# Performance work log

Measured on AMD Instinct MI355X. Metric: run time of the kernel, lower is better.

Reference implementation:

```python
import jax, jax.numpy as jnp
import numpy as np

WD, WH, WW = 2, 7, 7          # window size (d, h, w)
N = WD * WH * WW              # 98 tokens per window
DIM = 768
NH = 24
HD = DIM // NH                # 32
SCALE = HD ** -0.5
NW = 64                       # windows per image
B = 4
B_ = B * NW                   # 256


def _relative_position_index():
    d, h, w = np.meshgrid(np.arange(WD), np.arange(WH), np.arange(WW), indexing='ij')
    coords = np.stack([d.ravel(), h.ravel(), w.ravel()])        # (3, N)
    rel = (coords[:, :, None] - coords[:, None, :]).transpose(1, 2, 0)  # (N, N, 3)
    rel = rel + np.array([WD - 1, WH - 1, WW - 1])
    rel = rel * np.array([(2 * WH - 1) * (2 * WW - 1), 2 * WW - 1, 1])
    return rel.sum(-1).astype(np.int32)                         # (N, N)


def setup_inputs() -> dict:
    key = jax.random.key(0)
    ks = jax.random.split(key, 5)
    table_rows = (2 * WD - 1) * (2 * WH - 1) * (2 * WW - 1)     # 507
    return {
        'x': jax.random.normal(ks[0], (B_, N, DIM), jnp.float32),
        'mask': jax.random.normal(ks[1], (NW, N, N), jnp.float32),
        'qkv_w': jax.random.normal(ks[2], (3 * DIM, DIM), jnp.float32) * 0.02,
        'qkv_b': jax.random.normal(ks[3], (3 * DIM,), jnp.float32) * 0.02,
        'rel_table': jax.random.normal(ks[4], (table_rows, NH), jnp.float32) * 0.02,
        'rel_index': jnp.asarray(_relative_position_index()),
    }


def reference(x, mask, qkv_w, qkv_b, rel_table, rel_index):
    Bs, n, c = x.shape
    # qkv linear; einops '(nH hD qkv)' => last dim factored as (nH, hD, 3)
    qkv = x @ qkv_w.T + qkv_b                                   # (Bs, N, 3C)
    qkv = qkv.reshape(Bs, n, NH, HD, 3)
    q, k, v = (jnp.moveaxis(qkv, -1, 0)                         # (3, Bs, N, nH, hD)
                  .transpose(0, 1, 3, 2, 4))                    # (3, Bs, nH, N, hD)
    attn = jnp.einsum('bhqd,bhkd->bhqk', q, k) * SCALE          # (Bs, nH, N, N)
    bias = rel_table[rel_index]                                 # (N, N, nH)
    attn = attn + bias.transpose(2, 0, 1)[None]                 # + (1, nH, N, N)
    # window mask add
    attn = attn.reshape(Bs // NW, NW, NH, n, n) + mask[None, :, None]
    attn = attn.reshape(Bs, NH, n, n)
    attn = jax.nn.softmax(attn, axis=-1)
    out = jnp.einsum('bhqk,bhkd->bhqd', attn, v)                # (Bs, nH, N, hD)
    return out.transpose(0, 2, 1, 3).reshape(Bs, n, c)          # (Bs, N, C)
```

## Files before the change

kernel.cpp:

```cpp
#include <hip/hip_runtime.h>
#include <hip/hip_bf16.h>
#include <stdint.h>


#define NTOK 98
#define MT 7
#define NPAD 112
#define DIMX 768
#define NHEAD 24
#define HDIM 32
#define NQKV 2304
#define BROWS 25088
#define SCALE 0.17677669529663689f
#define LOG2E 1.4426950408889634f
#define SCL2E (SCALE * LOG2E)
#define NN2 (NTOK * NTOK)
#define BMROW 112
#define BMSZ (BMROW * BMROW)

#define NB_X 18816
#define NB_W 1728
#define NB_BM 18816

#if __has_builtin(__builtin_amdgcn_exp2f)
#define EXP2F(x) __builtin_amdgcn_exp2f(x)
#else
#define EXP2F(x) exp2f(x)
#endif

typedef __attribute__((ext_vector_type(8))) short short8;
typedef __attribute__((ext_vector_type(4))) short short4v;
typedef __attribute__((ext_vector_type(4))) float floatx4;

__device__ __forceinline__ short f2b(float f) {
    __hip_bfloat16 h = __float2bfloat16(f);
    return __builtin_bit_cast(short, h);
}
__device__ __forceinline__ float b2f(unsigned short s) {
    return __builtin_bit_cast(float, ((unsigned)s) << 16);
}

__device__ __forceinline__ void gload_lds16(const void* g, void* l) {
    __builtin_amdgcn_global_load_lds(
        (const __attribute__((address_space(1))) void*)g,
        (__attribute__((address_space(3))) void*)l, 16, 0, 0);
}

__device__ __forceinline__ void bm_body(int t,
                                        const float* __restrict__ rel_table,
                                        const int* __restrict__ rel_index,
                                        const float* __restrict__ mask,
                                        short* __restrict__ bm) {
    int wh = t / (BMSZ / 4);
    int r4 = t % (BMSZ / 4);
    int i = r4 / 28;
    int j0 = (r4 % 28) * 4;
    int h = wh % NHEAD, w = wh / NHEAD;
    short4v o;
    #pragma unroll
    for (int jj = 0; jj < 4; ++jj) {
        int j = j0 + jj;
        float val = -1e30f;
        if (i < NTOK && j < NTOK) {
            float bv = rel_table[(size_t)rel_index[i * NTOK + j] * NHEAD + h];
            float mv = mask[(size_t)w * NN2 + i * NTOK + j];
            val = (bv + mv) * LOG2E;
        }
        o[jj] = f2b(val);
    }
    *(short4v*)(bm + (size_t)wh * BMSZ + i * BMROW + j0) = o;
}

__global__ void prep_kernel(const float* __restrict__ x,
                            const float* __restrict__ w,
                            const float* __restrict__ rel_table,
                            const int* __restrict__ rel_index,
                            const float* __restrict__ mask,
                            short* __restrict__ xb,
                            short* __restrict__ wb,
                            short* __restrict__ bm) {
    int bid = blockIdx.x;
    if (bid < NB_X) {
        int i = bid * 256 + threadIdx.x;
        float4 f = ((const float4*)x)[i];
        short4v s = { f2b(f.x), f2b(f.y), f2b(f.z), f2b(f.w) };
        ((short4v*)xb)[i] = s;
    } else if (bid < NB_X + NB_W) {
        int i = (bid - NB_X) * 256 + threadIdx.x;
        int cp = i / 192, k4 = i % 192;
        int s = cp / DIMX, rem = cp % DIMX;
        int orig = (rem >> 5) * 96 + (rem & 31) * 3 + s;
        float sc = (s == 0) ? SCL2E : 1.0f;
        float4 f = ((const float4*)(w + (size_t)orig * DIMX))[k4];
        short4v o = { f2b(f.x * sc), f2b(f.y * sc), f2b(f.z * sc), f2b(f.w * sc) };
        ((short4v*)(wb + (size_t)cp * DIMX))[k4] = o;
    } else {
        int t = (bid - NB_X - NB_W) * 256 + threadIdx.x;
        bm_body(t, rel_table, rel_index, mask, bm);
    }
}

__global__ void bm_kernel(const float* __restrict__ rel_table,
                          const int* __restrict__ rel_index,
                          const float* __restrict__ mask,
                          short* __restrict__ bm) {
    int t = blockIdx.x * 256 + threadIdx.x;
    if (t >= 64 * NHEAD * BMSZ / 4) return;
    bm_body(t, rel_table, rel_index, mask, bm);
}

__global__ void bias_gather_kernel(const float* __restrict__ rel_table,
                                   const int* __restrict__ rel_index,
                                   float* __restrict__ bias_pre) {
    int t = blockIdx.x * 256 + threadIdx.x;
    if (t >= NHEAD * NN2) return;
    int h  = t / NN2;
    int ij = t % NN2;
    bias_pre[t] = rel_table[(size_t)rel_index[ij] * NHEAD + h];
}

__global__ void gemm_kernel(const short* __restrict__ xb,
                            const short* __restrict__ wb,
                            const float* __restrict__ qkv_b,
                            short* __restrict__ qkv) {
    __shared__ short At[128 * 64];
    __shared__ short Bt[128 * 64];
    const int tid  = threadIdx.x;
    const int lane = tid & 63;
    const int wv   = tid >> 6;
    const int wr   = wv >> 1, wc = wv & 1;
    const int l15  = lane & 15;
    const int l4   = lane >> 4;

    int bid = blockIdx.x;
    int swz = (bid & 7) * 441 + (bid >> 3);
    const int mtile = swz / 18;
    const int ntile = swz % 18;

    const short* aB = xb + (size_t)(mtile * 128) * DIMX;
    const short* bB = wb + (size_t)(ntile * 128) * DIMX;
    const int lrow = lane >> 3;
    const int lcs  = (((lane & 7) ^ lrow) * 8);
    const int sa   = (l15 & 7) << 3;

    floatx4 acc[4][4];
    #pragma unroll
    for (int m = 0; m < 4; ++m)
        #pragma unroll
        for (int n = 0; n < 4; ++n) acc[m][n] = (floatx4){0.f, 0.f, 0.f, 0.f};

    for (int kb = 0; kb < 12; ++kb) {
        #pragma unroll
        for (int j = 0; j < 4; ++j) {
            int r = wv * 32 + j * 8;
            gload_lds16(aB + (size_t)(r + lrow) * DIMX + kb * 64 + lcs, &At[r * 64]);
            gload_lds16(bB + (size_t)(r + lrow) * DIMX + kb * 64 + lcs, &Bt[r * 64]);
        }
        __syncthreads();
        #pragma unroll
        for (int kh = 0; kh < 2; ++kh) {
            int k0 = kh * 32 + l4 * 8;
            int k0s = k0 ^ sa;
            short8 af[4], bfr[4];
            #pragma unroll
            for (int m = 0; m < 4; ++m)
                af[m] = *(const short8*)(&At[(wr * 64 + m * 16 + l15) * 64 + k0s]);
            #pragma unroll
            for (int n = 0; n < 4; ++n)
                bfr[n] = *(const short8*)(&Bt[(wc * 64 + n * 16 + l15) * 64 + k0s]);
            #pragma unroll
            for (int m = 0; m < 4; ++m)
                #pragma unroll
                for (int n = 0; n < 4; ++n)
                    acc[m][n] = __builtin_amdgcn_mfma_f32_16x16x32_bf16(
                        af[m], bfr[n], acc[m][n], 0, 0, 0);
        }
        __syncthreads();
    }

    #pragma unroll
    for (int n = 0; n < 4; ++n) {
        int col = ntile * 128 + wc * 64 + n * 16 + l15;
        int s = col / DIMX, rem = col % DIMX;
        int orig = (rem >> 5) * 96 + (rem & 31) * 3 + s;
        float bias = qkv_b[orig] * ((s == 0) ? SCL2E : 1.0f);
        #pragma unroll
        for (int m = 0; m < 4; ++m) {
            int row0 = mtile * 128 + wr * 64 + m * 16 + l4 * 4;
            #pragma unroll
            for (int r = 0; r < 4; ++r)
                qkv[(size_t)(row0 + r) * NQKV + col] = f2b(acc[m][n][r] + bias);
        }
    }
}

struct __align__(16) SMemC {
    short P[NPAD * 128];
    short q[NPAD * HDIM];
    short k[NPAD * HDIM];
    short vt[HDIM * 128];
};

__global__ __launch_bounds__(256, 3) void attn_kernel4(
    const short* __restrict__ qkv,
    const short* __restrict__ bm,
    float* __restrict__ out) {
    __shared__ SMemC sm;
    const int tid  = threadIdx.x;
    const int lane = tid & 63;
    const int wv   = tid >> 6;
    const int l15  = lane & 15;
    const int l4   = lane >> 4;
    int id = blockIdx.x;
    int nb = (id & 7) * 768 + (id >> 3);
    const int b = nb / NHEAD;
    const int h = nb % NHEAD;
    const short* qbase = qkv + (size_t)b * NTOK * NQKV;

    #pragma unroll
    for (int it = 0; it < 2; ++it) {
        int row0 = it * 64 + wv * 16;
        if (row0 < NTOK) {
            int row = row0 + (lane >> 2);
            int seg = (lane & 3) * 8;
            if (row < NTOK) {
                gload_lds16(qbase + (size_t)row * NQKV + h * HDIM + seg,
                            &sm.q[row0 * HDIM]);
                gload_lds16(qbase + (size_t)row * NQKV + DIMX + h * HDIM + seg,
                            &sm.k[row0 * HDIM]);
            }
        }
    }
    if (tid < 196) {
        int t = (tid >> 2) * 2, dh = tid & 3;
        const short* vp = qbase + (size_t)t * NQKV + 2 * DIMX + h * HDIM + dh * 8;
        short8 va = *(const short8*)vp;
        short8 vb = *(const short8*)(vp + NQKV);
        #pragma unroll
        for (int j = 0; j < 8; ++j) {
            int d = dh * 8 + j;
            int csw = t ^ ((d & 7) << 3);
            unsigned pk = ((unsigned)(unsigned short)vb[j] << 16) |
                          (unsigned)(unsigned short)va[j];
            *(unsigned*)(&sm.vt[d * 128 + csw]) = pk;
        }
    }
    if (tid < 112) {
        int a = tid / 56, r2 = (tid % 56) >> 2, seg = (tid & 3) * 8;
        short* dst = (a ? sm.k : sm.q) + (NTOK + r2) * HDIM + seg;
        *(uint4*)dst = (uint4){0u, 0u, 0u, 0u};
    }
    for (int t = tid; t < HDIM * 30; t += 256) {
        int d = t / 30, c = NTOK + t % 30;
        sm.vt[d * 128 + (c ^ ((d & 7) << 3))] = 0;
    }
    for (int t = tid; t < NPAD * 16; t += 256) {
        int r = t >> 4, c = 112 + (t & 15);
        sm.P[r * 128 + (c ^ ((r & 7) << 3))] = 0;
    }
    __syncthreads();

    int mt[2];
    mt[0] = wv;
    mt[1] = (wv + 4 < MT) ? (wv + 4) : wv;

    floatx4 sacc[2][7];
    #pragma unroll
    for (int i = 0; i < 2; ++i)
        #pragma unroll
        for (int j = 0; j < 7; ++j) sacc[i][j] = (floatx4){0.f, 0.f, 0.f, 0.f};
    {
        int k0 = l4 * 8;
        short8 bq[2];
        #pragma unroll
        for (int iq = 0; iq < 2; ++iq)
            bq[iq] = *(const short8*)(&sm.q[(mt[iq] * 16 + l15) * HDIM + k0]);
        #pragma unroll
        for (int kt = 0; kt < 7; ++kt) {
            short8 ak = *(const short8*)(&sm.k[(kt * 16 + l15) * HDIM + k0]);
            #pragma unroll
            for (int iq = 0; iq < 2; ++iq)
                sacc[iq][kt] = __builtin_amdgcn_mfma_f32_16x16x32_bf16(
                    ak, bq[iq], sacc[iq][kt], 0, 0, 0);
        }
    }

    const short* bmh = bm + ((size_t)(b & 63) * NHEAD + h) * BMSZ;
    const int swzp = (l15 & 7) << 3;

    #pragma unroll
    for (int iq = 0; iq < 2; ++iq) {
        int q = mt[iq] * 16 + l15;
        const short* bmq = bmh + q * BMROW + l4 * 4;
        float vv[7][4];
        #pragma unroll
        for (int kt = 0; kt < 7; ++kt) {
            short4v bm4 = *(const short4v*)(bmq + kt * 16);
            #pragma unroll
            for (int r = 0; r < 4; ++r)
                vv[kt][r] = sacc[iq][kt][r] + b2f((unsigned short)bm4[r]);
        }
        float mx = vv[0][0];
        #pragma unroll
        for (int kt = 0; kt < 7; ++kt)
            #pragma unroll
            for (int r = 0; r < 4; ++r) mx = fmaxf(mx, vv[kt][r]);
        mx = fmaxf(mx, __shfl_xor(mx, 16));
        mx = fmaxf(mx, __shfl_xor(mx, 32));
        float s = 0.f;
        #pragma unroll
        for (int kt = 0; kt < 7; ++kt)
            #pragma unroll
            for (int r = 0; r < 4; ++r) {
                float e = EXP2F(vv[kt][r] - mx);
                vv[kt][r] = e;
                s += e;
            }
        s += __shfl_xor(s, 16);
        s += __shfl_xor(s, 32);
        float inv = (q < NTOK) ? 1.f / s : 0.f;
        #pragma unroll
        for (int kt = 0; kt < 7; ++kt) {
            short4v pw = { f2b(vv[kt][0] * inv), f2b(vv[kt][1] * inv),
                           f2b(vv[kt][2] * inv), f2b(vv[kt][3] * inv) };
            *(short4v*)(&sm.P[q * 128 + ((kt * 16 + l4 * 4) ^ swzp)]) = pw;
        }
    }
    __syncthreads();

    floatx4 oacc[2][2];
    #pragma unroll
    for (int i = 0; i < 2; ++i)
        #pragma unroll
        for (int j = 0; j < 2; ++j) oacc[i][j] = (floatx4){0.f, 0.f, 0.f, 0.f};

    #pragma unroll
    for (int kt = 0; kt < 4; ++kt) {
        int kk = (kt * 32 + l4 * 8) ^ swzp;
        short8 ap[2];
        #pragma unroll
        for (int im = 0; im < 2; ++im)
            ap[im] = *(const short8*)(&sm.P[(mt[im] * 16 + l15) * 128 + kk]);
        #pragma unroll
        for (int nt = 0; nt < 2; ++nt) {
            short8 bv = *(const short8*)(&sm.vt[(nt * 16 + l15) * 128 + kk]);
            #pragma unroll
            for (int im = 0; im < 2; ++im)
                oacc[im][nt] = __builtin_amdgcn_mfma_f32_16x16x32_bf16(
                    ap[im], bv, oacc[im][nt], 0, 0, 0);
        }
    }

    float* ob = out + (size_t)b * NTOK * DIMX + h * HDIM;
    #pragma unroll
    for (int im = 0; im < 2; ++im)
        #pragma unroll
        for (int nt = 0; nt < 2; ++nt) {
            int dd = nt * 16 + l15;
            #pragma unroll
            for (int r = 0; r < 4; ++r) {
                int tok = mt[im] * 16 + l4 * 4 + r;
                if (tok < NTOK)
                    ob[(size_t)tok * DIMX + dd] = oacc[im][nt][r];
            }
        }
}

struct __align__(16) SMemF {
    union {
        struct {
            short xt[NPAD * 64];
            short wt[96 * 64];
        } p1;
        short P[NPAD * 128];
    } u;
    short q[NPAD * HDIM];
    short k[NPAD * HDIM];
    short vt[HDIM * 128];
};

__global__ __launch_bounds__(256, 3) void attn_fused(
    const float* __restrict__ x,
    const float* __restrict__ mask,
    const float* __restrict__ qkv_w,
    const float* __restrict__ qkv_b,
    const float* __restrict__ bias_pre,
    const float* __restrict__ rel_table,
    const int* __restrict__ rel_index,
    float* __restrict__ out) {
    __shared__ SMemF sm;
    const int tid  = threadIdx.x;
    const int lane = tid & 63;
    const int wv   = tid >> 6;
    const int l15  = lane & 15;
    const int l4   = lane >> 4;
    const int b = blockIdx.x / NHEAD;
    const int h = blockIdx.x % NHEAD;
    const float* xp = x + (size_t)b * NTOK * DIMX;
    const float* wp = qkv_w + (size_t)h * 96 * DIMX;
    int mt[2];
    mt[0] = wv;
    mt[1] = (wv + 4 < MT) ? (wv + 4) : wv;

    floatx4 acc[2][6];
    #pragma unroll
    for (int i = 0; i < 2; ++i)
        #pragma unroll
        for (int j = 0; j < 6; ++j) acc[i][j] = (floatx4){0.f, 0.f, 0.f, 0.f};

    for (int kb = 0; kb < 12; ++kb) {
        for (int t = tid; t < NTOK * 16; t += 256) {
            int row = t >> 4, c = t & 15;
            float4 f = *(const float4*)(xp + (size_t)row * DIMX + kb * 64 + c * 4);
            short4v s = { f2b(f.x), f2b(f.y), f2b(f.z), f2b(f.w) };
            *(short4v*)(&sm.u.p1.xt[row * 64 + c * 4]) = s;
        }
        for (int t = tid; t < 96 * 16; t += 256) {
            int row = t >> 4, c = t & 15;
            float4 f = *(const float4*)(wp + (size_t)row * DIMX + kb * 64 + c * 4);
            short4v s = { f2b(f.x), f2b(f.y), f2b(f.z), f2b(f.w) };
            *(short4v*)(&sm.u.p1.wt[row * 64 + c * 4]) = s;
        }
        if (tid < 14 * 8) {
            int row = 98 + (tid >> 3), c = tid & 7;
            uint4 z = {0u, 0u, 0u, 0u};
            *(uint4*)(&sm.u.p1.xt[row * 64 + c * 8]) = z;
        }
        __syncthreads();
        #pragma unroll
        for (int ks = 0; ks < 2; ++ks) {
            int k0 = ks * 32 + l4 * 8;
            short8 aM[2];
            #pragma unroll
            for (int im = 0; im < 2; ++im)
                aM[im] = *(const short8*)(&sm.u.p1.xt[(mt[im] * 16 + l15) * 64 + k0]);
            #pragma unroll
            for (int nt = 0; nt < 6; ++nt) {
                short8 bN = *(const short8*)(&sm.u.p1.wt[(nt * 16 + l15) * 64 + k0]);
                #pragma unroll
                for (int im = 0; im < 2; ++im)
                    acc[im][nt] = __builtin_amdgcn_mfma_f32_16x16x32_bf16(
                        aM[im], bN, acc[im][nt], 0, 0, 0);
            }
        }
        __syncthreads();
    }

    #pragma unroll
    for (int im = 0; im < 2; ++im)
        #pragma unroll
        for (int nt = 0; nt < 6; ++nt) {
            int col = nt * 16 + l15;
            int d = col / 3, s = col % 3;
            float bias = qkv_b[h * 96 + col];
            #pragma unroll
            for (int r = 0; r < 4; ++r) {
                int tok = mt[im] * 16 + l4 * 4 + r;
                short val = f2b(acc[im][nt][r] + bias);
                if (s == 0)      sm.q[tok * HDIM + d] = val;
                else if (s == 1) sm.k[tok * HDIM + d] = val;
                else             sm.vt[d * 128 + tok] = val;
            }
        }
    __syncthreads();
    for (int t = tid; t < HDIM * 30; t += 256) {
        int d = t / 30, c = 98 + t % 30;
        sm.vt[d * 128 + c] = 0;
    }
    for (int t = tid; t < NPAD * 16; t += 256) {
        int row = t >> 4, c = 112 + (t & 15);
        sm.u.P[row * 128 + c] = 0;
    }

    floatx4 sacc[2][7];
    #pragma unroll
    for (int i = 0; i < 2; ++i)
        #pragma unroll
        for (int j = 0; j < 7; ++j) sacc[i][j] = (floatx4){0.f, 0.f, 0.f, 0.f};
    {
        int k0 = l4 * 8;
        short8 aq[2];
        #pragma unroll
        for (int im = 0; im < 2; ++im)
            aq[im] = *(const short8*)(&sm.q[(mt[im] * 16 + l15) * HDIM + k0]);
        #pragma unroll
        for (int nt = 0; nt < 7; ++nt) {
            short8 bk = *(const short8*)(&sm.k[(nt * 16 + l15) * HDIM + k0]);
            #pragma unroll
            for (int im = 0; im < 2; ++im)
                sacc[im][nt] = __builtin_amdgcn_mfma_f32_16x16x32_bf16(
                    aq[im], bk, sacc[im][nt], 0, 0, 0);
        }
    }

    const float* biash = bias_pre ? (bias_pre + (size_t)h * NN2) : nullptr;
    const size_t moff = (size_t)(b & 63) * NN2;

    #pragma unroll
    for (int im = 0; im < 2; ++im)
        #pragma unroll
        for (int r = 0; r < 4; ++r) {
            int row = mt[im] * 16 + l4 * 4 + r;
            bool vrow = row < NTOK;
            float v[7];
            #pragma unroll
            for (int nt = 0; nt < 7; ++nt) {
                int j = nt * 16 + l15;
                bool vj = vrow && (j < NTOK);
                float bmv = 0.f;
                if (vj) {
                    float bias = biash ? biash[row * NTOK + j]
                        : rel_table[(size_t)rel_index[row * NTOK + j] * NHEAD + h];
                    bmv = bias + mask[moff + row * NTOK + j];
                }
                v[nt] = vj ? sacc[im][nt][r] * SCALE + bmv : -1e30f;
            }
            float mx = v[0];
            #pragma unroll
            for (int nt = 1; nt < 7; ++nt) mx = fmaxf(mx, v[nt]);
            #pragma unroll
            for (int off = 1; off < 16; off <<= 1) mx = fmaxf(mx, __shfl_xor(mx, off));
            float s = 0.f;
            #pragma unroll
            for (int nt = 0; nt < 7; ++nt) {
                float e = (v[nt] > -1e29f) ? __expf(v[nt] - mx) : 0.f;
                v[nt] = e;
                s += e;
            }
            #pragma unroll
            for (int off = 1; off < 16; off <<= 1) s += __shfl_xor(s, off);
            float inv = vrow ? 1.f / s : 0.f;
            #pragma unroll
            for (int nt = 0; nt < 7; ++nt)
                sm.u.P[row * 128 + nt * 16 + l15] = f2b(v[nt] * inv);
        }
    __syncthreads();

    floatx4 oacc[2][2];
    #pragma unroll
    for (int i = 0; i < 2; ++i)
        #pragma unroll
        for (int j = 0; j < 2; ++j) oacc[i][j] = (floatx4){0.f, 0.f, 0.f, 0.f};
    #pragma unroll
    for (int kt = 0; kt < 4; ++kt) {
        int kk = kt * 32 + l4 * 8;
        short8 ap[2];
        #pragma unroll
        for (int im = 0; im < 2; ++im)
            ap[im] = *(const short8*)(&sm.u.P[(mt[im] * 16 + l15) * 128 + kk]);
        #pragma unroll
        for (int nt = 0; nt < 2; ++nt) {
            short8 bv = *(const short8*)(&sm.vt[(nt * 16 + l15) * 128 + kk]);
            #pragma unroll
            for (int im = 0; im < 2; ++im)
                oacc[im][nt] = __builtin_amdgcn_mfma_f32_16x16x32_bf16(
                    ap[im], bv, oacc[im][nt], 0, 0, 0);
        }
    }
    float* ob = out + (size_t)b * NTOK * DIMX + h * HDIM;
    #pragma unroll
    for (int im = 0; im < 2; ++im)
        #pragma unroll
        for (int nt = 0; nt < 2; ++nt) {
            int dd = nt * 16 + l15;
            #pragma unroll
            for (int r = 0; r < 4; ++r) {
                int tok = mt[im] * 16 + l4 * 4 + r;
                if (tok < NTOK)
                    ob[(size_t)tok * DIMX + dd] = oacc[im][nt][r];
            }
        }
}

extern "C" void kernel_launch(void* const* d_in, const int* in_sizes, int n_in,
                              void* d_out, int out_size, void* d_ws, size_t ws_size,
                              hipStream_t stream) {
    const float* x = (const float*)d_in[0];
    const float* mask = (const float*)d_in[1];
    const float* qkv_w = (const float*)d_in[2];
    const float* qkv_b = (const float*)d_in[3];
    const float* rel_table = (const float*)d_in[4];
    const int* rel_index = (const int*)d_in[5];
    for (int i = 0; i < n_in; ++i) {
        switch (in_sizes[i]) {
            case 256 * NTOK * DIMX:  x         = (const float*)d_in[i]; break;
            case 64 * NN2:           mask      = (const float*)d_in[i]; break;
            case 3 * DIMX * DIMX:    qkv_w     = (const float*)d_in[i]; break;
            case 3 * DIMX:           qkv_b     = (const float*)d_in[i]; break;
            case 507 * NHEAD:        rel_table = (const float*)d_in[i]; break;
            case NN2:                rel_index = (const int*)d_in[i]; break;
            default: break;
        }
    }
    float* out = (float*)d_out;

    const size_t xb_bytes   = (size_t)BROWS * DIMX * 2;
    const size_t wb_bytes   = (size_t)NQKV * DIMX * 2;
    const size_t qkv_bytes  = (size_t)BROWS * NQKV * 2;
    const size_t bm_bytes   = (size_t)64 * NHEAD * BMSZ * 2;
    const size_t total      = xb_bytes + wb_bytes + qkv_bytes;

    if (ws_size >= total) {
        short* xb  = (short*)d_ws;
        short* wb  = (short*)((char*)d_ws + xb_bytes);
        short* qkv = (short*)((char*)d_ws + xb_bytes + wb_bytes);

        if (ws_size >= total + bm_bytes) {
            short* bmp = (short*)((char*)d_ws + total);
            prep_kernel<<<NB_X + NB_W + NB_BM, 256, 0, stream>>>(
                x, qkv_w, rel_table, rel_index, mask, xb, wb, bmp);
            gemm_kernel<<<196 * 18, 256, 0, stream>>>(xb, wb, qkv_b, qkv);
            attn_kernel4<<<256 * NHEAD, 256, 0, stream>>>(qkv, bmp, out);
        } else {
            short* bmp = (short*)d_ws;
            prep_kernel<<<NB_X + NB_W, 256, 0, stream>>>(
                x, qkv_w, rel_table, rel_index, mask, xb, wb, nullptr);
            gemm_kernel<<<196 * 18, 256, 0, stream>>>(xb, wb, qkv_b, qkv);
            int nbm = 64 * NHEAD * BMSZ / 4;
            bm_kernel<<<(nbm + 255) / 256, 256, 0, stream>>>(
                rel_table, rel_index, mask, bmp);
            attn_kernel4<<<256 * NHEAD, 256, 0, stream>>>(qkv, bmp, out);
        }
    } else {
        const size_t bias_bytes = (size_t)NHEAD * NN2 * sizeof(float);
        float* bias_pre = (ws_size >= bias_bytes) ? (float*)d_ws : nullptr;
        if (bias_pre) {
            int nb = NHEAD * NN2;
            bias_gather_kernel<<<(nb + 255) / 256, 256, 0, stream>>>(rel_table, rel_index, bias_pre);
        }
        attn_fused<<<256 * NHEAD, 256, 0, stream>>>(x, mask, qkv_w, qkv_b,
                                                    bias_pre, rel_table, rel_index, out);
    }
}
```

Measured before the change: 347.2 us.

## Store QKV head-planar, fold bias-mask build into GEMM launch, raise MFMA priority

The GEMM epilogue now writes Q, K and V into per-head contiguous planes (s, head, row, d) instead of interleaved rows of width 2304. The attention kernel therefore loads each head's 98x32 tile as contiguous memory, replacing strided row gathers. The bias+mask table build moves from the prep kernel into extra blocks of the GEMM launch, so it runs alongside the GEMM tiles. s_setprio is raised around the MFMA loops in attention. The risk is that the epilogue stores now stride 64 bytes per row, which may coalesce worse, and the GEMM tail may be lengthened by the bm blocks.

```diff
diff --git a/kernel.cpp b/kernel.cpp
--- a/kernel.cpp
+++ b/kernel.cpp
@@ -17,10 +17,12 @@
 #define NN2 (NTOK * NTOK)
 #define BMROW 112
 #define BMSZ (BMROW * BMROW)
+#define PLANE ((size_t)BROWS * HDIM)
 
 #define NB_X 18816
 #define NB_W 1728
 #define NB_BM 18816
+#define GEMM_BLKS 3528
 
 #if __has_builtin(__builtin_amdgcn_exp2f)
 #define EXP2F(x) __builtin_amdgcn_exp2f(x)
@@ -73,19 +75,15 @@
 
 __global__ void prep_kernel(const float* __restrict__ x,
                             const float* __restrict__ w,
-                            const float* __restrict__ rel_table,
-                            const int* __restrict__ rel_index,
-                            const float* __restrict__ mask,
                             short* __restrict__ xb,
-                            short* __restrict__ wb,
-                            short* __restrict__ bm) {
+                            short* __restrict__ wb) {
     int bid = blockIdx.x;
     if (bid < NB_X) {
         int i = bid * 256 + threadIdx.x;
         float4 f = ((const float4*)x)[i];
         short4v s = { f2b(f.x), f2b(f.y), f2b(f.z), f2b(f.w) };
         ((short4v*)xb)[i] = s;
-    } else if (bid < NB_X + NB_W) {
+    } else {
         int i = (bid - NB_X) * 256 + threadIdx.x;
         int cp = i / 192, k4 = i % 192;
         int s = cp / DIMX, rem = cp % DIMX;
@@ -94,9 +92,6 @@
         float4 f = ((const float4*)(w + (size_t)orig * DIMX))[k4];
         short4v o = { f2b(f.x * sc), f2b(f.y * sc), f2b(f.z * sc), f2b(f.w * sc) };
         ((short4v*)(wb + (size_t)cp * DIMX))[k4] = o;
-    } else {
-        int t = (bid - NB_X - NB_W) * 256 + threadIdx.x;
-        bm_body(t, rel_table, rel_index, mask, bm);
     }
 }
 
@@ -122,7 +117,16 @@
 __global__ void gemm_kernel(const short* __restrict__ xb,
                             const short* __restrict__ wb,
                             const float* __restrict__ qkv_b,
-                            short* __restrict__ qkv) {
+                            short* __restrict__ qkv,
+                            const float* __restrict__ rel_table,
+                            const int* __restrict__ rel_index,
+                            const float* __restrict__ mask,
+                            short* __restrict__ bm) {
+    if (blockIdx.x >= GEMM_BLKS) {
+        int t = (blockIdx.x - GEMM_BLKS) * 256 + threadIdx.x;
+        bm_body(t, rel_table, rel_index, mask, bm);
+        return;
+    }
     __shared__ short At[128 * 64];
     __shared__ short Bt[128 * 64];
     const int tid  = threadIdx.x;
@@ -182,14 +186,16 @@
     for (int n = 0; n < 4; ++n) {
         int col = ntile * 128 + wc * 64 + n * 16 + l15;
         int s = col / DIMX, rem = col % DIMX;
-        int orig = (rem >> 5) * 96 + (rem & 31) * 3 + s;
+        int h2 = rem >> 5, d = rem & 31;
+        int orig = h2 * 96 + d * 3 + s;
         float bias = qkv_b[orig] * ((s == 0) ? SCL2E : 1.0f);
+        short* base = qkv + (size_t)(s * NHEAD + h2) * PLANE + d;
         #pragma unroll
         for (int m = 0; m < 4; ++m) {
             int row0 = mtile * 128 + wr * 64 + m * 16 + l4 * 4;
             #pragma unroll
             for (int r = 0; r < 4; ++r)
-                qkv[(size_t)(row0 + r) * NQKV + col] = f2b(acc[m][n][r] + bias);
+                base[(size_t)(row0 + r) * HDIM] = f2b(acc[m][n][r] + bias);
         }
     }
 }
@@ -201,7 +207,7 @@
     short vt[HDIM * 128];
 };
 
-__global__ __launch_bounds__(256, 3) void attn_kernel4(
+__global__ __launch_bounds__(256, 3) void attn_kernel5(
     const short* __restrict__ qkv,
     const short* __restrict__ bm,
     float* __restrict__ out) {
@@ -215,27 +221,25 @@
     int nb = (id & 7) * 768 + (id >> 3);
     const int b = nb / NHEAD;
     const int h = nb % NHEAD;
-    const short* qbase = qkv + (size_t)b * NTOK * NQKV;
+    const short* qh = qkv + (size_t)h * PLANE            + (size_t)b * NTOK * HDIM;
+    const short* kh = qkv + (size_t)(NHEAD + h) * PLANE  + (size_t)b * NTOK * HDIM;
+    const short* vh = qkv + (size_t)(2 * NHEAD + h) * PLANE + (size_t)b * NTOK * HDIM;
 
     #pragma unroll
     for (int it = 0; it < 2; ++it) {
         int row0 = it * 64 + wv * 16;
         if (row0 < NTOK) {
-            int row = row0 + (lane >> 2);
-            int seg = (lane & 3) * 8;
-            if (row < NTOK) {
-                gload_lds16(qbase + (size_t)row * NQKV + h * HDIM + seg,
-                            &sm.q[row0 * HDIM]);
-                gload_lds16(qbase + (size_t)row * NQKV + DIMX + h * HDIM + seg,
-                            &sm.k[row0 * HDIM]);
+            if (lane < (NTOK - row0) * 4) {
+                gload_lds16(qh + row0 * HDIM + lane * 8, &sm.q[row0 * HDIM]);
+                gload_lds16(kh + row0 * HDIM + lane * 8, &sm.k[row0 * HDIM]);
             }
         }
     }
     if (tid < 196) {
         int t = (tid >> 2) * 2, dh = tid & 3;
-        const short* vp = qbase + (size_t)t * NQKV + 2 * DIMX + h * HDIM + dh * 8;
+        const short* vp = vh + t * HDIM + dh * 8;
         short8 va = *(const short8*)vp;
-        short8 vb = *(const short8*)(vp + NQKV);
+        short8 vb = *(const short8*)(vp + HDIM);
         #pragma unroll
         for (int j = 0; j < 8; ++j) {
             int d = dh * 8 + j;
@@ -275,6 +279,7 @@
         #pragma unroll
         for (int iq = 0; iq < 2; ++iq)
             bq[iq] = *(const short8*)(&sm.q[(mt[iq] * 16 + l15) * HDIM + k0]);
+        __builtin_amdgcn_s_setprio(1);
         #pragma unroll
         for (int kt = 0; kt < 7; ++kt) {
             short8 ak = *(const short8*)(&sm.k[(kt * 16 + l15) * HDIM + k0]);
@@ -283,6 +288,7 @@
                 sacc[iq][kt] = __builtin_amdgcn_mfma_f32_16x16x32_bf16(
                     ak, bq[iq], sacc[iq][kt], 0, 0, 0);
         }
+        __builtin_amdgcn_s_setprio(0);
     }
 
     const short* bmh = bm + ((size_t)(b & 63) * NHEAD + h) * BMSZ;
@@ -334,6 +340,7 @@
         #pragma unroll
         for (int j = 0; j < 2; ++j) oacc[i][j] = (floatx4){0.f, 0.f, 0.f, 0.f};
 
+    __builtin_amdgcn_s_setprio(1);
     #pragma unroll
     for (int kt = 0; kt < 4; ++kt) {
         int kk = (kt * 32 + l4 * 8) ^ swzp;
@@ -350,6 +357,7 @@
                     ap[im], bv, oacc[im][nt], 0, 0, 0);
         }
     }
+    __builtin_amdgcn_s_setprio(0);
 
     float* ob = out + (size_t)b * NTOK * DIMX + h * HDIM;
     #pragma unroll
@@ -605,21 +613,20 @@
         short* wb  = (short*)((char*)d_ws + xb_bytes);
         short* qkv = (short*)((char*)d_ws + xb_bytes + wb_bytes);
 
+        prep_kernel<<<NB_X + NB_W, 256, 0, stream>>>(x, qkv_w, xb, wb);
         if (ws_size >= total + bm_bytes) {
             short* bmp = (short*)((char*)d_ws + total);
-            prep_kernel<<<NB_X + NB_W + NB_BM, 256, 0, stream>>>(
-                x, qkv_w, rel_table, rel_index, mask, xb, wb, bmp);
-            gemm_kernel<<<196 * 18, 256, 0, stream>>>(xb, wb, qkv_b, qkv);
-            attn_kernel4<<<256 * NHEAD, 256, 0, stream>>>(qkv, bmp, out);
+            gemm_kernel<<<GEMM_BLKS + NB_BM, 256, 0, stream>>>(
+                xb, wb, qkv_b, qkv, rel_table, rel_index, mask, bmp);
+            attn_kernel5<<<256 * NHEAD, 256, 0, stream>>>(qkv, bmp, out);
         } else {
             short* bmp = (short*)d_ws;
-            prep_kernel<<<NB_X + NB_W, 256, 0, stream>>>(
-                x, qkv_w, rel_table, rel_index, mask, xb, wb, nullptr);
-            gemm_kernel<<<196 * 18, 256, 0, stream>>>(xb, wb, qkv_b, qkv);
+            gemm_kernel<<<GEMM_BLKS, 256, 0, stream>>>(
+                xb, wb, qkv_b, qkv, rel_table, rel_index, mask, nullptr);
             int nbm = 64 * NHEAD * BMSZ / 4;
             bm_kernel<<<(nbm + 255) / 256, 256, 0, stream>>>(
                 rel_table, rel_index, mask, bmp);
-            attn_kernel4<<<256 * NHEAD, 256, 0, stream>>>(qkv, bmp, out);
+            attn_kernel5<<<256 * NHEAD, 256, 0, stream>>>(qkv, bmp, out);
         }
     } else {
         const size_t bias_bytes = (size_t)NHEAD * NN2 * sizeof(float);
```

After: 340.4 us. -2.0%, faster.
